# Kernel tuning notes

Hardware: AMD Instinct MI355X
Metric: run time of the kernel (lower is better)

The kernel has to match this reference:

```python
import jax, jax.numpy as jnp
import numpy as np

N_NODES = 50000
N_EDGES = 800000
D = 64  # all feature sizes


def setup_inputs() -> dict:
    key = jax.random.key(0)
    ks = jax.random.split(key, 16)

    def unif(k, shape, fan_out):
        stdv = 0.2 / np.sqrt(fan_out)
        return jax.random.uniform(k, shape, jnp.float32, -stdv, stdv)

    return {
        "Skipnode_in_feats": jax.random.normal(ks[0], (N_NODES, D), jnp.float32),
        "node_in_feats": jax.random.normal(ks[1], (N_NODES, D), jnp.float32),
        "edge_in_feats": jax.random.normal(ks[2], (N_EDGES, D), jnp.float32),
        "src": jax.random.randint(ks[3], (N_EDGES,), 0, N_NODES, jnp.int32),
        "dst": jax.random.randint(ks[4], (N_EDGES,), 0, N_NODES, jnp.int32),
        "weight_n2n_u": unif(ks[5], (D, D), D),
        "weight_n2n_v": unif(ks[6], (3 * D, D), D),
        "weight_e2n": unif(ks[7], (D, D), D),
        "bias_n": unif(ks[8], (D,), D),
        "weight_n2e_u": unif(ks[9], (D, D), D),
        "weight_n2e_v": unif(ks[10], (2 * D, D), D),
        "weight_e2e": unif(ks[11], (2 * D, D), D),
        "bias_e": unif(ks[12], (D,), D),
    }


def reference(Skipnode_in_feats, node_in_feats, edge_in_feats, src, dst,
              weight_n2n_u, weight_n2n_v, weight_e2n, bias_n,
              weight_n2e_u, weight_n2e_v, weight_e2e, bias_e):
    n_nodes = node_in_feats.shape[0]

    # node -> node messages: m_e = (X W_u)[src] + (E W_e2n)[e], mean over dst
    h1 = node_in_feats @ weight_n2n_u            # [N, D]
    e1 = edge_in_feats @ weight_e2n              # [E, D]
    m = h1[src] + e1                             # [E, D]
    summed = jax.ops.segment_sum(m, dst, num_segments=n_nodes)          # [N, D]
    deg = jax.ops.segment_sum(jnp.ones_like(dst, jnp.float32), dst,
                              num_segments=n_nodes)                     # [N]
    h_neigh = summed / jnp.maximum(deg, 1.0)[:, None]  # DGL mean: 0 for isolated

    h_total = jnp.concatenate([Skipnode_in_feats, node_in_feats, h_neigh], axis=1)
    h_out = h_total @ weight_n2n_v + bias_n      # [N, D]

    # edge update: e2 = (X W_n2e_u)[src] + ([S,X] W_n2e_v)[dst]
    hu = node_in_feats @ weight_n2e_u            # [N, D]
    hc = jnp.concatenate([Skipnode_in_feats, node_in_feats], axis=1)
    hv = hc @ weight_n2e_v                       # [N, D]
    e2 = hu[src] + hv[dst]                       # [E, D]
    e_total = jnp.concatenate([edge_in_feats, e2], axis=1)
    e_out = e_total @ weight_e2e + bias_e        # [E, D]

    return (h_out, e_out)
```

## Files before the change

kernel.cpp:

```cpp
#include <hip/hip_runtime.h>

#define N_NODES 50000
#define N_EDGES 800000
#define D 64
#define ET_PAD 68
#define NB 196

typedef __attribute__((ext_vector_type(8))) short short8;
typedef __attribute__((ext_vector_type(4))) float f32x4;

__device__ inline unsigned short f2bf(float f) {
    unsigned u = __float_as_uint(f);
    unsigned r = (u + 0x7FFFu + ((u >> 16) & 1u)) >> 16;
    return (unsigned short)r;
}

__global__ void fold_weights(const float* __restrict__ w_n2n_u,
                             const float* __restrict__ w_n2n_v,
                             const float* __restrict__ w_e2n,
                             const float* __restrict__ w_n2e_u,
                             const float* __restrict__ w_n2e_v,
                             const float* __restrict__ w_e2e,
                             float* __restrict__ Wbig,
                             unsigned short* __restrict__ WTbf) {
    int bidx = blockIdx.x;
    int j = threadIdx.x;
    const float* Ebot = w_e2e + 64 * 64;
    const float* Wv3  = w_n2n_v + 128 * 64;
    if (bidx < 512) {
        int k = bidx >> 2, q = bidx & 3;
        float v = 0.f;
        if (q == 0) {
            v = w_n2n_v[k * 64 + j];
        } else if (q == 1) {
            if (k >= 64) for (int t = 0; t < 64; ++t) v = fmaf(w_n2e_u[(k - 64) * 64 + t], Ebot[t * 64 + j], v);
        } else if (q == 2) {
            for (int t = 0; t < 64; ++t) v = fmaf(w_n2e_v[k * 64 + t], Ebot[t * 64 + j], v);
        } else {
            if (k >= 64) for (int t = 0; t < 64; ++t) v = fmaf(w_n2n_u[(k - 64) * 64 + t], Wv3[t * 64 + j], v);
        }
        Wbig[(size_t)k * 256 + q * 64 + j] = v;
    } else if (bidx < 576) {
        int k = bidx - 512;
        float v = 0.f;
        for (int t = 0; t < 64; ++t) v = fmaf(w_e2n[k * 64 + t], Wv3[t * 64 + j], v);
        WTbf[(64 + j) * 64 + k] = f2bf(v);
    } else {
        int k = bidx - 576;
        WTbf[j * 64 + k] = f2bf(w_e2e[k * 64 + j]);
    }
}

__global__ __launch_bounds__(256) void node_pre(
    const float* __restrict__ S, const float* __restrict__ X,
    const float* __restrict__ Wbig, const float* __restrict__ bias_n,
    float* __restrict__ h_out, float* __restrict__ AX, float* __restrict__ bvec) {
    __shared__ __align__(16) float inT[64 * ET_PAD];
    __shared__ __align__(16) float Wl[64 * 64];
    const int t = threadIdx.x;
    const int m0 = blockIdx.x * 64, q = blockIdx.y, c0 = q * 64;
    const int tx = t & 15, ty = t >> 4;
    float acc[4][4] = {{0.f}};
    for (int h = 0; h < 2; ++h) {
        const float* P = h ? X : S;
        #pragma unroll
        for (int i = 0; i < 16; ++i) {
            int idx = i * 256 + t;
            int ml = idx >> 6, kl = idx & 63;
            int m = m0 + ml;
            inT[kl * ET_PAD + ml] = (m < N_NODES) ? P[(size_t)m * 64 + kl] : 0.f;
        }
        #pragma unroll
        for (int i = 0; i < 16; ++i) {
            int idx = i * 256 + t;
            int kl = idx >> 6, jl = idx & 63;
            Wl[kl * 64 + jl] = Wbig[(size_t)(h * 64 + kl) * 256 + c0 + jl];
        }
        __syncthreads();
        #pragma unroll 4
        for (int kl = 0; kl < 64; ++kl) {
            float4 av = *(const float4*)&inT[kl * ET_PAD + ty * 4];
            float4 wv = *(const float4*)&Wl[kl * 64 + tx * 4];
            float a4[4] = {av.x, av.y, av.z, av.w};
            float w4[4] = {wv.x, wv.y, wv.z, wv.w};
            #pragma unroll
            for (int im = 0; im < 4; ++im)
                #pragma unroll
                for (int ij = 0; ij < 4; ++ij)
                    acc[im][ij] = fmaf(a4[im], w4[ij], acc[im][ij]);
        }
        __syncthreads();
    }
    #pragma unroll
    for (int im = 0; im < 4; ++im) {
        int m = m0 + ty * 4 + im;
        if (m >= N_NODES) continue;
        #pragma unroll
        for (int ij = 0; ij < 4; ++ij) {
            int jl = tx * 4 + ij;
            float v = acc[im][ij];
            if (q == 0)      h_out[(size_t)m * 64 + jl] = v + bias_n[jl];
            else if (q == 1) AX[(size_t)m * 128 + 2 * jl] = v;
            else if (q == 2) bvec[(size_t)m * 64 + jl] = v;
            else             AX[(size_t)m * 128 + 2 * jl + 1] = v;
        }
    }
}

__global__ void hist_k(const int* __restrict__ dst, int* __restrict__ counts) {
    int e = blockIdx.x * 256 + threadIdx.x;
    if (e < N_EDGES) atomicAdd(&counts[dst[e]], 1);
}

__global__ void scan1(const int* __restrict__ counts, int* __restrict__ bsum) {
    __shared__ int s[256];
    int t = threadIdx.x;
    int i = blockIdx.x * 256 + t;
    s[t] = (i < N_NODES) ? counts[i] : 0;
    __syncthreads();
    for (int off = 128; off > 0; off >>= 1) {
        if (t < off) s[t] += s[t + off];
        __syncthreads();
    }
    if (t == 0) bsum[blockIdx.x] = s[0];
}

__global__ void scan2(const int* __restrict__ bsum, int* __restrict__ boff) {
    __shared__ int s[256];
    int t = threadIdx.x;
    int v0 = (t < NB) ? bsum[t] : 0;
    s[t] = v0;
    __syncthreads();
    for (int off = 1; off < 256; off <<= 1) {
        int v = (t >= off) ? s[t - off] : 0;
        __syncthreads();
        s[t] += v;
        __syncthreads();
    }
    if (t < NB) boff[t] = s[t] - v0;
}

__global__ void scan3(const int* __restrict__ counts, const int* __restrict__ boff,
                      int* __restrict__ offsets, int* __restrict__ cursor) {
    __shared__ int s[256];
    int t = threadIdx.x;
    int i = blockIdx.x * 256 + t;
    int v0 = (i < N_NODES) ? counts[i] : 0;
    s[t] = v0;
    __syncthreads();
    for (int off = 1; off < 256; off <<= 1) {
        int v = (t >= off) ? s[t - off] : 0;
        __syncthreads();
        s[t] += v;
        __syncthreads();
    }
    int excl = s[t] - v0 + boff[blockIdx.x];
    if (i < N_NODES) { offsets[i] = excl; cursor[i] = excl; }
    if (i == N_NODES - 1) offsets[N_NODES] = excl + v0;
}

__global__ void scatter_k(const int* __restrict__ src, const int* __restrict__ dst,
                          int* __restrict__ cursor, int4* __restrict__ sEdge) {
    int e = blockIdx.x * 256 + threadIdx.x;
    if (e < N_EDGES) {
        int d = dst[e];
        int p = atomicAdd(&cursor[d], 1);
        sEdge[p] = make_int4(e, src[e], d, 0);
    }
}

__global__ __launch_bounds__(256) void edge_kernel(
    const float* __restrict__ E, const int4* __restrict__ sEdge,
    const unsigned short* __restrict__ WTbf,
    const float* __restrict__ AX, const float* __restrict__ bvec,
    const float* __restrict__ bias_e,
    float* __restrict__ e_out, float* __restrict__ hpre) {
    __shared__ __align__(16) unsigned short sEt[64 * 64];
    __shared__ __align__(16) float sOut[64 * 128];

    const int t = threadIdx.x;
    const int lane = t & 63;
    const int w = t >> 6;
    const int p0 = blockIdx.x * 64;
    const int l15 = lane & 15, qd = lane >> 4;
    const int j = lane;

    float2 axv[16];
    float  bv[16];
    int    permv[16], dstv[16];
    #pragma unroll
    for (int r = 0; r < 16; ++r) {
        int4 ed = sEdge[p0 + 16 * w + r];
        permv[r] = ed.x;
        dstv[r]  = ed.z;
        axv[r] = *(const float2*)&AX[(size_t)ed.y * 128 + 2 * j];
        bv[r]  = bvec[(size_t)ed.z * 64 + j];
    }

    #pragma unroll
    for (int i = 0; i < 8; ++i) {
        int idx = i * 64 + lane;
        int r  = idx >> 5;
        int kp = idx & 31;
        int pe = sEdge[p0 + 16 * w + r].x;
        float2 ev = *(const float2*)&E[(size_t)pe * 64 + 2 * kp];
        unsigned pk = ((unsigned)f2bf(ev.y) << 16) | (unsigned)f2bf(ev.x);
        *(unsigned*)&sEt[(16 * w + r) * 64 + 2 * kp] = pk;
    }

    const short8 a0 = *(const short8*)&sEt[(16 * w + l15) * 64 +  0 + qd * 8];
    const short8 a1 = *(const short8*)&sEt[(16 * w + l15) * 64 + 32 + qd * 8];
    #pragma unroll
    for (int tt = 0; tt < 8; ++tt) {
        const short8 b0 = *(const short8*)&WTbf[(16 * tt + l15) * 64 +  0 + qd * 8];
        const short8 b1 = *(const short8*)&WTbf[(16 * tt + l15) * 64 + 32 + qd * 8];
        f32x4 d = {0.f, 0.f, 0.f, 0.f};
        d = __builtin_amdgcn_mfma_f32_16x16x32_bf16(a0, b0, d, 0, 0, 0);
        d = __builtin_amdgcn_mfma_f32_16x16x32_bf16(a1, b1, d, 0, 0, 0);
        int colw = (tt < 4) ? (16 * tt + l15) : (16 * (tt - 4) + l15);
        int pos  = (tt < 4) ? (2 * colw) : (2 * colw + 1);
        #pragma unroll
        for (int reg = 0; reg < 4; ++reg)
            sOut[(16 * w + qd * 4 + reg) * 128 + pos] = d[reg];
    }

    const float bj = bias_e[j];
    float acc2[16];
    #pragma unroll
    for (int r = 0; r < 16; ++r) {
        float2 o = *(const float2*)&sOut[(16 * w + r) * 128 + 2 * j];
        float v1 = o.x + bj + axv[r].x + bv[r];
        acc2[r]  = o.y + axv[r].y;
        e_out[(size_t)permv[r] * 64 + j] = v1;
    }

    int cur = dstv[0];
    float run = acc2[0];
    #pragma unroll
    for (int r = 1; r < 16; ++r) {
        if (dstv[r] == cur) {
            run += acc2[r];
        } else {
            atomicAdd(&hpre[(size_t)cur * 64 + j], run);
            cur = dstv[r];
            run = acc2[r];
        }
    }
    atomicAdd(&hpre[(size_t)cur * 64 + j], run);
}

__global__ void node_final(float* __restrict__ h_out,
                           const float* __restrict__ hpre,
                           const int* __restrict__ offsets) {
    int i = blockIdx.x * blockDim.x + threadIdx.x;
    if (i < N_NODES * 64) {
        int n = i >> 6;
        float deg = (float)(offsets[n + 1] - offsets[n]);
        float r = 1.0f / fmaxf(deg, 1.0f);
        h_out[i] += hpre[i] * r;
    }
}

extern "C" void kernel_launch(void* const* d_in, const int* in_sizes, int n_in,
                              void* d_out, int out_size, void* d_ws, size_t ws_size,
                              hipStream_t stream) {
    const float* S       = (const float*)d_in[0];
    const float* X       = (const float*)d_in[1];
    const float* E       = (const float*)d_in[2];
    const int*   src     = (const int*)  d_in[3];
    const int*   dst     = (const int*)  d_in[4];
    const float* w_n2n_u = (const float*)d_in[5];
    const float* w_n2n_v = (const float*)d_in[6];
    const float* w_e2n   = (const float*)d_in[7];
    const float* bias_n  = (const float*)d_in[8];
    const float* w_n2e_u = (const float*)d_in[9];
    const float* w_n2e_v = (const float*)d_in[10];
    const float* w_e2e   = (const float*)d_in[11];
    const float* bias_e  = (const float*)d_in[12];

    const size_t ND = (size_t)N_NODES * 64;

    float* ws = (float*)d_ws;
    float*          hpre    = ws;
    float*          AX      = ws + ND;
    float*          bvec    = AX + (size_t)N_NODES * 128;
    float*          Wbig    = bvec + ND;
    unsigned short* WTbf    = (unsigned short*)(Wbig + 128 * 256);
    int*            counts  = (int*)(WTbf + 8192);
    int4*           sEdge   = (int4*)(counts + N_NODES);
    int*            offsets = (int*)(sEdge + N_EDGES);
    int*            cursor  = offsets + N_NODES + 1;
    int*            bsum    = cursor + N_NODES;
    int*            boff    = bsum + 200;

    float* h_out = (float*)d_out;
    float* e_out = h_out + ND;

    hipMemsetAsync(hpre, 0, ND * sizeof(float), stream);
    hipMemsetAsync(counts, 0, N_NODES * sizeof(int), stream);

    fold_weights<<<640, 64, 0, stream>>>(w_n2n_u, w_n2n_v, w_e2n, w_n2e_u,
                                         w_n2e_v, w_e2e, Wbig, WTbf);

    dim3 npGrid((N_NODES + 63) / 64, 4);
    node_pre<<<npGrid, 256, 0, stream>>>(S, X, Wbig, bias_n, h_out, AX, bvec);

    hist_k <<<(N_EDGES + 255) / 256, 256, 0, stream>>>(dst, counts);
    scan1  <<<NB, 256, 0, stream>>>(counts, bsum);
    scan2  <<<1, 256, 0, stream>>>(bsum, boff);
    scan3  <<<NB, 256, 0, stream>>>(counts, boff, offsets, cursor);
    scatter_k<<<(N_EDGES + 255) / 256, 256, 0, stream>>>(src, dst, cursor, sEdge);

    edge_kernel<<<N_EDGES / 64, 256, 0, stream>>>(
        E, sEdge, WTbf, AX, bvec, bias_e, e_out, hpre);

    node_final<<<(N_NODES * 64 + 255) / 256, 256, 0, stream>>>(h_out, hpre, offsets);
}
```

Before: 724.8 us.

## Compute transposed MFMA in registers, drop LDS staging, segmented shuffle scan for atomics

Reworks the edge kernel so each lane loads its own edge row directly into registers, converts it to bf16 and swaps the MFMA operands so the output lands with edges on lanes and features in registers. This removes both shared-memory buffers, the LDS transpose and the output staging, and switches global reads and writes to 16-byte vector accesses. The per-destination reduction becomes a segmented shuffle scan within 16-lane groups, and only segment tails issue atomics. The scan is still correct, but it adds shuffle work, and each tail lane now makes four scalar atomics to nearby addresses, which changes the atomic access pattern.

```diff
diff --git a/kernel.cpp b/kernel.cpp
--- a/kernel.cpp
+++ b/kernel.cpp
@@ -175,78 +175,94 @@
     const float* __restrict__ AX, const float* __restrict__ bvec,
     const float* __restrict__ bias_e,
     float* __restrict__ e_out, float* __restrict__ hpre) {
-    __shared__ __align__(16) unsigned short sEt[64 * 64];
-    __shared__ __align__(16) float sOut[64 * 128];
-
     const int t = threadIdx.x;
     const int lane = t & 63;
     const int w = t >> 6;
-    const int p0 = blockIdx.x * 64;
     const int l15 = lane & 15, qd = lane >> 4;
-    const int j = lane;
-
-    float2 axv[16];
-    float  bv[16];
-    int    permv[16], dstv[16];
+
+    int4 ed = sEdge[blockIdx.x * 64 + 16 * w + l15];
+    const int perm = ed.x, srcn = ed.y, dstn = ed.z;
+
+    const float* Erow = E + (size_t)perm * 64 + qd * 8;
+    f32x4 e00 = *(const f32x4*)(Erow);
+    f32x4 e01 = *(const f32x4*)(Erow + 4);
+    f32x4 e10 = *(const f32x4*)(Erow + 32);
+    f32x4 e11 = *(const f32x4*)(Erow + 36);
+
+    const float* AXr = AX + (size_t)srcn * 128 + 8 * qd;
+    f32x4 ax0[4], ax1[4];
     #pragma unroll
-    for (int r = 0; r < 16; ++r) {
-        int4 ed = sEdge[p0 + 16 * w + r];
-        permv[r] = ed.x;
-        dstv[r]  = ed.z;
-        axv[r] = *(const float2*)&AX[(size_t)ed.y * 128 + 2 * j];
-        bv[r]  = bvec[(size_t)ed.z * 64 + j];
-    }
-
+    for (int u = 0; u < 4; ++u) {
+        ax0[u] = *(const f32x4*)(AXr + 32 * u);
+        ax1[u] = *(const f32x4*)(AXr + 32 * u + 4);
+    }
+
+    short8 eb0, eb1;
     #pragma unroll
-    for (int i = 0; i < 8; ++i) {
-        int idx = i * 64 + lane;
-        int r  = idx >> 5;
-        int kp = idx & 31;
-        int pe = sEdge[p0 + 16 * w + r].x;
-        float2 ev = *(const float2*)&E[(size_t)pe * 64 + 2 * kp];
-        unsigned pk = ((unsigned)f2bf(ev.y) << 16) | (unsigned)f2bf(ev.x);
-        *(unsigned*)&sEt[(16 * w + r) * 64 + 2 * kp] = pk;
-    }
-
-    const short8 a0 = *(const short8*)&sEt[(16 * w + l15) * 64 +  0 + qd * 8];
-    const short8 a1 = *(const short8*)&sEt[(16 * w + l15) * 64 + 32 + qd * 8];
+    for (int jj = 0; jj < 4; ++jj) {
+        eb0[jj]     = (short)f2bf(e00[jj]);
+        eb0[jj + 4] = (short)f2bf(e01[jj]);
+        eb1[jj]     = (short)f2bf(e10[jj]);
+        eb1[jj + 4] = (short)f2bf(e11[jj]);
+    }
+
+    const int k1 = __shfl_up(dstn, 1, 16);
+    const int k2 = __shfl_up(dstn, 2, 16);
+    const int k4 = __shfl_up(dstn, 4, 16);
+    const int k8 = __shfl_up(dstn, 8, 16);
+    const int nd = __shfl_down(dstn, 1, 16);
+    const bool p1 = (l15 >= 1) && (k1 == dstn);
+    const bool p2 = (l15 >= 2) && (k2 == dstn);
+    const bool p4 = (l15 >= 4) && (k4 == dstn);
+    const bool p8 = (l15 >= 8) && (k8 == dstn);
+    const bool tail = (l15 == 15) || (nd != dstn);
+
+    const unsigned short* Wt = WTbf + l15 * 64 + qd * 8;
+
     #pragma unroll
     for (int tt = 0; tt < 8; ++tt) {
-        const short8 b0 = *(const short8*)&WTbf[(16 * tt + l15) * 64 +  0 + qd * 8];
-        const short8 b1 = *(const short8*)&WTbf[(16 * tt + l15) * 64 + 32 + qd * 8];
+        short8 wt0 = *(const short8*)(Wt + tt * 16 * 64);
+        short8 wt1 = *(const short8*)(Wt + tt * 16 * 64 + 32);
         f32x4 d = {0.f, 0.f, 0.f, 0.f};
-        d = __builtin_amdgcn_mfma_f32_16x16x32_bf16(a0, b0, d, 0, 0, 0);
-        d = __builtin_amdgcn_mfma_f32_16x16x32_bf16(a1, b1, d, 0, 0, 0);
-        int colw = (tt < 4) ? (16 * tt + l15) : (16 * (tt - 4) + l15);
-        int pos  = (tt < 4) ? (2 * colw) : (2 * colw + 1);
-        #pragma unroll
-        for (int reg = 0; reg < 4; ++reg)
-            sOut[(16 * w + qd * 4 + reg) * 128 + pos] = d[reg];
-    }
-
-    const float bj = bias_e[j];
-    float acc2[16];
-    #pragma unroll
-    for (int r = 0; r < 16; ++r) {
-        float2 o = *(const float2*)&sOut[(16 * w + r) * 128 + 2 * j];
-        float v1 = o.x + bj + axv[r].x + bv[r];
-        acc2[r]  = o.y + axv[r].y;
-        e_out[(size_t)permv[r] * 64 + j] = v1;
-    }
-
-    int cur = dstv[0];
-    float run = acc2[0];
-    #pragma unroll
-    for (int r = 1; r < 16; ++r) {
-        if (dstv[r] == cur) {
-            run += acc2[r];
+        d = __builtin_amdgcn_mfma_f32_16x16x32_bf16(wt0, eb0, d, 0, 0, 0);
+        d = __builtin_amdgcn_mfma_f32_16x16x32_bf16(wt1, eb1, d, 0, 0, 0);
+        if (tt < 4) {
+            f32x4 bsv = *(const f32x4*)(bias_e + 16 * tt + 4 * qd);
+            f32x4 bvv = *(const f32x4*)(bvec + (size_t)dstn * 64 + 16 * tt + 4 * qd);
+            f32x4 o;
+            o[0] = d[0] + ax0[tt][0];
+            o[1] = d[1] + ax0[tt][2];
+            o[2] = d[2] + ax1[tt][0];
+            o[3] = d[3] + ax1[tt][2];
+            o += bsv + bvv;
+            *(f32x4*)(e_out + (size_t)perm * 64 + 16 * tt + 4 * qd) = o;
         } else {
-            atomicAdd(&hpre[(size_t)cur * 64 + j], run);
-            cur = dstv[r];
-            run = acc2[r];
-        }
-    }
-    atomicAdd(&hpre[(size_t)cur * 64 + j], run);
+            const int u = tt - 4;
+            float v0 = d[0] + ax0[u][1];
+            float v1 = d[1] + ax0[u][3];
+            float v2 = d[2] + ax1[u][1];
+            float v3 = d[3] + ax1[u][3];
+            { float o0 = __shfl_up(v0, 1, 16), o1 = __shfl_up(v1, 1, 16),
+                    o2 = __shfl_up(v2, 1, 16), o3 = __shfl_up(v3, 1, 16);
+              if (p1) { v0 += o0; v1 += o1; v2 += o2; v3 += o3; } }
+            { float o0 = __shfl_up(v0, 2, 16), o1 = __shfl_up(v1, 2, 16),
+                    o2 = __shfl_up(v2, 2, 16), o3 = __shfl_up(v3, 2, 16);
+              if (p2) { v0 += o0; v1 += o1; v2 += o2; v3 += o3; } }
+            { float o0 = __shfl_up(v0, 4, 16), o1 = __shfl_up(v1, 4, 16),
+                    o2 = __shfl_up(v2, 4, 16), o3 = __shfl_up(v3, 4, 16);
+              if (p4) { v0 += o0; v1 += o1; v2 += o2; v3 += o3; } }
+            { float o0 = __shfl_up(v0, 8, 16), o1 = __shfl_up(v1, 8, 16),
+                    o2 = __shfl_up(v2, 8, 16), o3 = __shfl_up(v3, 8, 16);
+              if (p8) { v0 += o0; v1 += o1; v2 += o2; v3 += o3; } }
+            if (tail) {
+                float* hp = hpre + (size_t)dstn * 64 + 16 * u + 4 * qd;
+                atomicAdd(hp + 0, v0);
+                atomicAdd(hp + 1, v1);
+                atomicAdd(hp + 2, v2);
+                atomicAdd(hp + 3, v3);
+            }
+        }
+    }
 }
 
 __global__ void node_final(float* __restrict__ h_out,
```

Result: slower. 747.4 us (+3.1%).
